# Performance work log

Measured on AMD Instinct MI355X. Metric: run time of the kernel, lower is better.

Reference implementation:

```python
import jax, jax.numpy as jnp
import numpy as np

DIM = 2048
NUM_HEADS = 16
NUM_KV_HEADS = 4
HEAD_DIM = DIM // NUM_HEADS  # 128
ROPE_BASE = 10000.0
CLIP = 31.0
BLOCK = 128


def fake_quant(w):
    """Blockwise int-ish fake quantization, steady QAT state (ratio=1, clip=31, no noise)."""
    out_f, in_f = w.shape
    pad = (-in_f) % BLOCK
    wp = jnp.pad(w, ((0, 0), (0, pad)))
    wb = wp.reshape(-1, BLOCK)
    # scale computed under no_grad in torch -> stop_gradient
    bmax = jnp.max(jnp.abs(wb), axis=1)
    s = jnp.maximum(bmax / CLIP, 1e-12).astype(jnp.float16)
    s = jnp.maximum(s, jnp.finfo(jnp.float16).tiny).astype(jnp.float32)
    s = jax.lax.stop_gradient(s)[:, None]
    ws = wb / s
    q = ws - jax.lax.stop_gradient(ws) + jax.lax.stop_gradient(
        jnp.round(jnp.clip(ws, -(CLIP + 1.0), CLIP)))  # STE
    qw = (q * s).reshape(out_f, in_f + pad)
    return qw[:, :in_f] if pad > 0 else qw


def rms_norm(x):
    eps = jnp.finfo(x.dtype).eps
    return x * jax.lax.rsqrt(jnp.mean(x * x, axis=-1, keepdims=True) + eps)


def rope_tables(seqlen, dtype):
    inv_freq = 1.0 / (ROPE_BASE ** (jnp.arange(0, HEAD_DIM, 2, dtype=jnp.float32) / HEAD_DIM))
    freqs = jnp.outer(jnp.arange(seqlen, dtype=jnp.float32), inv_freq)  # [S, hd/2]
    return jnp.cos(freqs).astype(dtype), jnp.sin(freqs).astype(dtype)


def apply_rotary(x, cos, sin):
    # x: [B,H,S,hd]; cos/sin: [S,hd/2]
    half = x.shape[-1] // 2
    x1, x2 = x[..., :half], x[..., half:]
    return jnp.concatenate((x1 * cos + x2 * sin, -x1 * sin + x2 * cos), axis=-1)


def setup_inputs() -> dict:
    key = jax.random.key(0)
    ks = jax.random.split(key, 6)
    kv_dim = NUM_KV_HEADS * HEAD_DIM
    std = DIM ** -0.5
    return {
        "x": jax.random.normal(ks[0], (2, 2048, DIM), dtype=jnp.float32),
        "Wq": jax.random.normal(ks[1], (DIM, DIM), dtype=jnp.float32) * std,
        "Wk": jax.random.normal(ks[2], (kv_dim, DIM), dtype=jnp.float32) * std,
        "Wv": jax.random.normal(ks[3], (kv_dim, DIM), dtype=jnp.float32) * std,
        "Wproj": jax.random.normal(ks[4], (DIM, DIM), dtype=jnp.float32) * std,
        "q_gain": jnp.full((NUM_HEADS,), 1.0, dtype=jnp.float32),
    }


def reference(x, Wq, Wk, Wv, Wproj, q_gain):
    B, S, D = x.shape
    H, KV, hd = NUM_HEADS, NUM_KV_HEADS, HEAD_DIM
    q = (x @ fake_quant(Wq).T).reshape(B, S, H, hd).transpose(0, 2, 1, 3)   # [B,H,S,hd]
    k = (x @ fake_quant(Wk).T).reshape(B, S, KV, hd).transpose(0, 2, 1, 3)  # [B,KV,S,hd]
    v = (x @ fake_quant(Wv).T).reshape(B, S, KV, hd).transpose(0, 2, 1, 3)
    q = rms_norm(q)
    k = rms_norm(k)
    cos, sin = rope_tables(S, q.dtype)
    q = apply_rotary(q, cos, sin)
    k = apply_rotary(k, cos, sin)
    q = q * q_gain[None, :, None, None]
    # GQA: expand kv heads
    rep = H // KV
    k = jnp.repeat(k, rep, axis=1)  # [B,H,S,hd]
    v = jnp.repeat(v, rep, axis=1)
    scale = 1.0 / jnp.sqrt(jnp.asarray(hd, dtype=q.dtype))
    scores = jnp.einsum("bhqd,bhkd->bhqk", q, k) * scale
    causal = jnp.tril(jnp.ones((S, S), dtype=bool))
    scores = jnp.where(causal, scores, jnp.asarray(-jnp.inf, dtype=scores.dtype))
    attn = jax.nn.softmax(scores, axis=-1)
    y = jnp.einsum("bhqk,bhkd->bhqd", attn, v)  # [B,H,S,hd]
    y = y.transpose(0, 2, 1, 3).reshape(B, S, D)
    return y @ fake_quant(Wproj).T
```

## Files before the change

kernel.cpp:

```cpp
#include <hip/hip_runtime.h>
#include <hip/hip_bf16.h>
#include <hip/hip_fp16.h>

#define SEQ    2048
#define DMODEL 2048
#define NH     16
#define NKV    4
#define HD     128
#define NTOT   3072
#define MROWS  4096

typedef __attribute__((ext_vector_type(4))) float f32x4;
typedef __attribute__((ext_vector_type(8))) __bf16 bf16x8;
typedef __attribute__((ext_vector_type(8))) unsigned short u16x8;
typedef __attribute__((ext_vector_type(4))) unsigned short u16x4;

__device__ __forceinline__ void async_copy16(const void* g, void* l) {
  __builtin_amdgcn_global_load_lds(
      (const __attribute__((address_space(1))) void*)g,
      (__attribute__((address_space(3))) void*)l, 16, 0, 0);
}

__device__ __forceinline__ unsigned short fto16(float f) {
  __hip_bfloat16 h = __float2bfloat16(f);
  return *(unsigned short*)&h;
}

__device__ __forceinline__ float b2f(unsigned short u) {
  unsigned int t = (unsigned int)u << 16;
  float f;
  __builtin_memcpy(&f, &t, 4);
  return f;
}

#define QSCALE 0.12751791437524245f
#define NEG_L2RB_64 (-0.2076205059304601f)

#define NFQ   20480
#define NCONV 8192
#define NROPE 512
__global__ __launch_bounds__(256) void prep_kernel(const float* __restrict__ Wq,
                                                   const float* __restrict__ Wk,
                                                   const float* __restrict__ Wv,
                                                   const float* __restrict__ Wp,
                                                   const float* __restrict__ x,
                                                   unsigned short* __restrict__ Wcat,
                                                   unsigned short* __restrict__ Wpq,
                                                   unsigned short* __restrict__ xb,
                                                   float* __restrict__ CS,
                                                   float* __restrict__ SN) {
  const int bid = blockIdx.x;
  const int tid = threadIdx.x;
  if (bid < NFQ) {
    int g = bid * 4 + (tid >> 6);
    int lane = tid & 63;
    const float* W;
    unsigned short* out;
    int blk;
    if (g < 32768)      { W = Wq; out = Wcat;                          blk = g; }
    else if (g < 40960) { W = Wk; out = Wcat + (size_t)2048 * 2048;    blk = g - 32768; }
    else if (g < 49152) { W = Wv; out = Wcat + (size_t)2560 * 2048;    blk = g - 40960; }
    else                { W = Wp; out = Wpq;                           blk = g - 49152; }
    const float* p = W + (size_t)blk * 128 + lane * 2;
    float w0 = p[0], w1 = p[1];
    float m = fmaxf(fabsf(w0), fabsf(w1));
#pragma unroll
    for (int o = 32; o; o >>= 1) m = fmaxf(m, __shfl_xor(m, o));
    float s = fmaxf(m / 31.0f, 1e-12f);
    s = __half2float(__float2half(s));
    s = fmaxf(s, 6.103515625e-05f);
    float q0 = rintf(fminf(fmaxf(w0 / s, -32.0f), 31.0f)) * s;
    float q1 = rintf(fminf(fmaxf(w1 / s, -32.0f), 31.0f)) * s;
    unsigned short* o16 = out + (size_t)blk * 128 + lane * 2;
    o16[0] = fto16(q0);
    o16[1] = fto16(q1);
  } else if (bid < NFQ + NCONV) {
    int i = ((bid - NFQ) * 256 + tid) * 4;
    float4 v = *(const float4*)(x + i);
    ushort4 o;
    o.x = fto16(v.x); o.y = fto16(v.y); o.z = fto16(v.z); o.w = fto16(v.w);
    *(ushort4*)(xb + i) = o;
  } else {
    int idx = (bid - NFQ - NCONV) * 256 + tid;
    int t = idx >> 6, l = idx & 63;
    float invf = exp2f((float)l * NEG_L2RB_64);
    float fr = (float)t * invf;
    CS[idx] = cosf(fr);
    SN[idx] = sinf(fr);
  }
}

#define BM 128
#define BN 128
#define BK 64
template <typename OT, bool FUSED>
__global__ __launch_bounds__(256, 3) void gemm_bt(const unsigned short* __restrict__ A,
                                                  const unsigned short* __restrict__ Bm,
                                                  OT* __restrict__ C,
                                                  unsigned short* __restrict__ vtb,
                                                  unsigned short* __restrict__ qbuf,
                                                  unsigned short* __restrict__ kbuf,
                                                  const float* __restrict__ qgain,
                                                  const float* __restrict__ CS,
                                                  const float* __restrict__ SN,
                                                  int M, int N, int K) {
  __shared__ unsigned short SH[FUSED ? 16896 : 16384];
  unsigned short* As = SH;
  unsigned short* Bs = SH + 8192;
  const int tid = threadIdx.x;
  const int wave = tid >> 6, lane = tid & 63;
  const int quad = lane >> 4, l16 = lane & 15;

  int wg = blockIdx.y * gridDim.x + blockIdx.x;
  int nwg = gridDim.x * gridDim.y;
  int cpx = nwg >> 3;
  int swz = (wg & 7) * cpx + (wg >> 3);
  int bxs = swz % gridDim.x, bys = swz / gridDim.x;
  const int m0 = bxs * BM, n0 = bys * BN;
  const int wm = (wave >> 1) * 64, wn = (wave & 1) * 64;

  const unsigned short* Ag = A + (size_t)m0 * K;
  const unsigned short* Bg = Bm + (size_t)n0 * K;

  f32x4 acc[4][4];
#pragma unroll
  for (int i = 0; i < 4; i++)
#pragma unroll
    for (int j = 0; j < 4; j++) acc[i][j] = f32x4{0.f, 0.f, 0.f, 0.f};

  const int srow = tid >> 3;
  const int sg8 = (((lane & 7) ^ (lane >> 3))) * 8;
  const unsigned short* gA = Ag + (size_t)srow * K + sg8;
  const unsigned short* gB = Bg + (size_t)srow * K + sg8;
  unsigned short* lA = &As[wave * 512];
  unsigned short* lB = &Bs[wave * 512];

  for (int k0 = 0; k0 < K; k0 += BK) {
    __syncthreads();
#pragma unroll
    for (int c = 0; c < 4; ++c) async_copy16(gA + (size_t)c * 32 * K + k0, lA + c * 2048);
#pragma unroll
    for (int c = 0; c < 4; ++c) async_copy16(gB + (size_t)c * 32 * K + k0, lB + c * 2048);
    __syncthreads();
#pragma unroll
    for (int kk = 0; kk < 2; ++kk) {
      bf16x8 af[4], bf[4];
#pragma unroll
      for (int t = 0; t < 4; t++)
        af[t] = *(const bf16x8*)&As[(wm + t * 16 + l16) * BK + ((((kk << 2) + quad) ^ (l16 & 7)) << 3)];
#pragma unroll
      for (int t = 0; t < 4; t++)
        bf[t] = *(const bf16x8*)&Bs[(wn + t * 16 + l16) * BK + ((((kk << 2) + quad) ^ (l16 & 7)) << 3)];
#pragma unroll
      for (int i = 0; i < 4; i++)
#pragma unroll
        for (int j = 0; j < 4; j++)
          acc[i][j] = __builtin_amdgcn_mfma_f32_16x16x32_bf16(af[i], bf[j], acc[i][j], 0, 0, 0);
    }
  }

  if constexpr (FUSED) {
    if (n0 >= 2560) {
      const int kvh = (n0 - 2560) >> 7;
#pragma unroll
      for (int i = 0; i < 4; i++) {
        int row0 = m0 + wm + i * 16 + quad * 4;
        int bz = row0 >> 11, s0 = row0 & 2047;
#pragma unroll
        for (int j = 0; j < 4; j++) {
          int d = wn + j * 16 + l16;
          u16x4 o;
#pragma unroll
          for (int r = 0; r < 4; r++) o[r] = fto16(acc[i][j][r]);
          *(u16x4*)&vtb[(size_t)((bz * NKV + kvh) * HD + d) * SEQ + s0] = o;
        }
      }
      return;
    }
    __syncthreads();
#pragma unroll
    for (int i = 0; i < 4; i++) {
      int tok0 = wm + i * 16 + quad * 4;
#pragma unroll
      for (int j = 0; j < 4; j++) {
        int d = wn + j * 16 + l16;
        u16x4 w;
#pragma unroll
        for (int r = 0; r < 4; r++) w[r] = fto16(acc[i][j][r]);
        *(u16x4*)&SH[d * 132 + tok0] = w;
      }
    }
    __syncthreads();
    const bool isq = (n0 < 2048);
    const int hh = isq ? (n0 >> 7) : ((n0 - 2048) >> 7);
    const float g = isq ? qgain[hh] * QSCALE : 1.0f;
#pragma unroll 1
    for (int gr = 0; gr < 8; ++gr) {
      int tk = wave * 32 + gr * 4;
      u16x4 a = *(const u16x4*)&SH[lane * 132 + tk];
      u16x4 b = *(const u16x4*)&SH[(lane + 64) * 132 + tk];
      float x1[4], x2[4], ss[4];
#pragma unroll
      for (int r = 0; r < 4; r++) {
        x1[r] = b2f(a[r]); x2[r] = b2f(b[r]);
        ss[r] = x1[r] * x1[r] + x2[r] * x2[r];
      }
#pragma unroll
      for (int o = 32; o; o >>= 1)
#pragma unroll
        for (int r = 0; r < 4; r++) ss[r] += __shfl_xor(ss[r], o);
#pragma unroll
      for (int r = 0; r < 4; r++) {
        int gt = m0 + tk + r;
        int bz = gt >> 11, tokg = gt & 2047;
        float rn = rsqrtf(ss[r] * (1.0f / 128.0f) + 1.1920929e-07f);
        float cs = CS[tokg * 64 + lane], sn = SN[tokg * 64 + lane];
        float n1 = x1[r] * rn, n2 = x2[r] * rn;
        unsigned short* dst = isq
            ? qbuf + ((size_t)(bz * NH + hh) * SEQ + tokg) * HD
            : kbuf + ((size_t)(bz * NKV + hh) * SEQ + tokg) * HD;
        dst[lane]      = fto16((n1 * cs + n2 * sn) * g);
        dst[lane + 64] = fto16((-n1 * sn + n2 * cs) * g);
      }
    }
    return;
  }

#pragma unroll
  for (int i = 0; i < 4; i++) {
    int row_base = m0 + wm + i * 16 + quad * 4;
#pragma unroll
    for (int j = 0; j < 4; j++) {
      int col = n0 + wn + j * 16 + l16;
#pragma unroll
      for (int r = 0; r < 4; r++) {
        if constexpr (sizeof(OT) == 2)
          C[(size_t)(row_base + r) * N + col] = fto16(acc[i][j][r]);
        else
          C[(size_t)(row_base + r) * N + col] = acc[i][j][r];
      }
    }
  }
}

__global__ __launch_bounds__(512, 4) void attn_kernel(const unsigned short* __restrict__ qb,
                                                      const unsigned short* __restrict__ kb,
                                                      const unsigned short* __restrict__ vtb,
                                                      unsigned short* __restrict__ yb,
                                                      float* __restrict__ Opart,
                                                      float* __restrict__ mlb) {
  __shared__ unsigned short Ks[2][64 * 128];
  __shared__ unsigned short Vt[128 * 64];
  __shared__ unsigned short Ps[8][16 * 64];

  const int bx = blockIdx.x;
  const int h = blockIdx.y;
  const int bz = blockIdx.z;
  const int tid = threadIdx.x;
  const int wave = tid >> 6, lane = tid & 63;
  const int quad = lane >> 4, l16 = lane & 15;

  int qt, k0, k1, cchunk = -1, qi = 0;
  if (bx < 12) {
    qt = bz ? bx : (11 - bx);
    k0 = 0; k1 = 2 * qt + 2;
  } else {
    int idx = bx - 12;
    qi = idx >> 1; cchunk = idx & 1;
    qt = 12 + qi;
    int nkt = 2 * qt + 2, half = nkt >> 1;
    k0 = cchunk ? half : 0;
    k1 = cchunk ? nkt : half;
  }

  const int base = qt * 128 + wave * 16;
  const int kdiag = base >> 6;

  const unsigned short* qg = qb + (size_t)(bz * NH + h) * SEQ * HD;
  const unsigned short* kg = kb + (size_t)(bz * NKV + (h >> 2)) * SEQ * HD;
  const unsigned short* vg = vtb + (size_t)(bz * NKV + (h >> 2)) * HD * SEQ;
  unsigned short* psw = &Ps[wave][0];

  bf16x8 qf[4];
#pragma unroll
  for (int ds = 0; ds < 4; ++ds)
    qf[ds] = *(const bf16x8*)(qg + (size_t)(base + l16) * HD + ds * 32 + quad * 8);

  f32x4 oacc[8];
#pragma unroll
  for (int j = 0; j < 8; ++j) oacc[j] = f32x4{0.f, 0.f, 0.f, 0.f};
  float m_i = -__builtin_inff();
  float l_i = 0.f;

  const int krow0 = wave * 4 + (lane >> 4);
  const int ksrcg = (lane & 15) ^ (krow0 & 15);
  const unsigned short* kgK = kg + (size_t)krow0 * HD + ksrcg * 8;

  const int vdw = tid >> 3, vgr = tid & 7;

  async_copy16(kgK + (size_t)k0 * 64 * HD, &Ks[k0 & 1][wave * 512]);
  async_copy16(kgK + (size_t)(k0 * 64 + 32) * HD, &Ks[k0 & 1][4096 + wave * 512]);
  u16x8 pv[2];
#pragma unroll
  for (int i = 0; i < 2; ++i)
    pv[i] = *(const u16x8*)(vg + (size_t)(i * 64 + vdw) * SEQ + k0 * 64 + vgr * 8);

  for (int kt = k0; kt < k1; ++kt) {
    __syncthreads();
#pragma unroll
    for (int i = 0; i < 2; ++i) {
      int d = i * 64 + vdw;
      *(u16x8*)&Vt[d * 64 + ((vgr ^ (d & 7)) << 3)] = pv[i];
    }
    if (kt + 1 < k1) {
      const unsigned short* s = kgK + (size_t)(kt + 1) * 64 * HD;
      async_copy16(s, &Ks[(kt + 1) & 1][wave * 512]);
      async_copy16(s + (size_t)32 * HD, &Ks[(kt + 1) & 1][4096 + wave * 512]);
    }
    __asm__ volatile("s_waitcnt lgkmcnt(0)" ::: "memory");
    __builtin_amdgcn_sched_barrier(0);
    __asm__ volatile("s_barrier" ::: "memory");

    if (kt + 1 < k1) {
#pragma unroll
      for (int i = 0; i < 2; ++i)
        pv[i] = *(const u16x8*)(vg + (size_t)(i * 64 + vdw) * SEQ + (kt + 1) * 64 + vgr * 8);
    }

    if (kt <= kdiag) {
      const unsigned short* Kc = Ks[kt & 1];
      f32x4 st[4];
#pragma unroll
      for (int mt = 0; mt < 4; ++mt) st[mt] = f32x4{0.f, 0.f, 0.f, 0.f};
      __builtin_amdgcn_s_setprio(1);
#pragma unroll
      for (int mt = 0; mt < 4; ++mt)
#pragma unroll
        for (int ds = 0; ds < 4; ++ds) {
          bf16x8 kf = *(const bf16x8*)&Kc[(mt * 16 + l16) * 128 + ((((ds << 2) + quad) ^ l16) << 3)];
          st[mt] = __builtin_amdgcn_mfma_f32_16x16x32_bf16(kf, qf[ds], st[mt], 0, 0, 0);
        }
      __builtin_amdgcn_s_setprio(0);

      const int qrow = base + l16;
      float p[4][4];
      float mx = -__builtin_inff();
      if (kt == kdiag) {
#pragma unroll
        for (int mt = 0; mt < 4; ++mt)
#pragma unroll
          for (int r = 0; r < 4; ++r) {
            int kp = kt * 64 + mt * 16 + quad * 4 + r;
            float v = (kp <= qrow) ? st[mt][r] : -__builtin_inff();
            p[mt][r] = v;
            mx = fmaxf(mx, v);
          }
      } else {
#pragma unroll
        for (int mt = 0; mt < 4; ++mt)
#pragma unroll
          for (int r = 0; r < 4; ++r) {
            p[mt][r] = st[mt][r];
            mx = fmaxf(mx, st[mt][r]);
          }
      }
      mx = fmaxf(mx, __shfl_xor(mx, 16));
      mx = fmaxf(mx, __shfl_xor(mx, 32));
      float mnew = (mx > m_i + 8.f) ? mx : m_i;
      float rs = 0.f;
#pragma unroll
      for (int mt = 0; mt < 4; ++mt)
#pragma unroll
        for (int r = 0; r < 4; ++r) {
          float e = exp2f(p[mt][r] - mnew);
          p[mt][r] = e;
          rs += e;
        }
      rs += __shfl_xor(rs, 16);
      rs += __shfl_xor(rs, 32);
      if (mnew != m_i) {
        float a = exp2f(m_i - mnew);
#pragma unroll
        for (int j = 0; j < 8; ++j) oacc[j] *= a;
        l_i = l_i * a + rs;
        m_i = mnew;
      } else {
        l_i += rs;
      }

#pragma unroll
      for (int mt = 0; mt < 4; ++mt) {
        u16x4 w;
#pragma unroll
        for (int r = 0; r < 4; ++r) w[r] = fto16(p[mt][r]);
        int g = mt * 2 + (quad >> 1);
        *(u16x4*)&psw[l16 * 64 + ((g ^ (l16 & 7)) << 3) + (quad & 1) * 4] = w;
      }

      __asm__ volatile("s_waitcnt lgkmcnt(0)" ::: "memory");

      __builtin_amdgcn_s_setprio(1);
#pragma unroll
      for (int c = 0; c < 2; ++c) {
        bf16x8 pf = *(const bf16x8*)&psw[l16 * 64 + ((((c << 2) + quad) ^ (l16 & 7)) << 3)];
#pragma unroll
        for (int mt = 0; mt < 8; ++mt) {
          bf16x8 vf = *(const bf16x8*)&Vt[(mt * 16 + l16) * 64 + ((((c << 2) + quad) ^ (l16 & 7)) << 3)];
          oacc[mt] = __builtin_amdgcn_mfma_f32_16x16x32_bf16(vf, pf, oacc[mt], 0, 0, 0);
        }
      }
      __builtin_amdgcn_s_setprio(0);
    }
  }

  if (cchunk >= 0) {
    const int rloc = wave * 16 + l16;
    float* op = Opart + ((size_t)(((cchunk * 2 + bz) * NH + h) * 4 + qi) * 128 + rloc) * 128;
#pragma unroll
    for (int mt = 0; mt < 8; ++mt)
      *(f32x4*)&op[mt * 16 + quad * 4] = oacc[mt];
    if (quad == 0) {
      float* ml = mlb + (size_t)(((cchunk * 2 + bz) * NH + h) * 4 + qi) * 256;
      ml[rloc] = m_i;
      ml[128 + rloc] = l_i;
    }
    return;
  }

  {
    float il = 1.0f / l_i;
    int qrow = base + l16;
#pragma unroll
    for (int mt = 0; mt < 8; ++mt) {
      u16x4 o;
#pragma unroll
      for (int r = 0; r < 4; ++r) o[r] = fto16(oacc[mt][r] * il);
      *(u16x4*)&yb[(size_t)(bz * SEQ + qrow) * DMODEL + h * HD + mt * 16 + quad * 4] = o;
    }
  }
}

__global__ __launch_bounds__(256) void combine_kernel(const float* __restrict__ Opart,
                                                      const float* __restrict__ mlb,
                                                      unsigned short* __restrict__ yb) {
  const int qi = blockIdx.x & 3;
  const int h = (blockIdx.x >> 2) & 15;
  const int bz = blockIdx.x >> 6;
  const int q = threadIdx.x >> 1;
  const int dh = (threadIdx.x & 1) * 64;

  const size_t i0 = (size_t)(((0 * 2 + bz) * NH + h) * 4 + qi);
  const size_t i1 = (size_t)(((1 * 2 + bz) * NH + h) * 4 + qi);
  const float m1 = mlb[i0 * 256 + q],     l1 = mlb[i0 * 256 + 128 + q];
  const float m2 = mlb[i1 * 256 + q],     l2 = mlb[i1 * 256 + 128 + q];
  const float mm = fmaxf(m1, m2);
  float w1 = exp2f(m1 - mm), w2 = exp2f(m2 - mm);
  const float il = 1.0f / (l1 * w1 + l2 * w2);
  w1 *= il; w2 *= il;

  const float* o1 = Opart + (i0 * 128 + q) * 128;
  const float* o2 = Opart + (i1 * 128 + q) * 128;
  const int qrow = (12 + qi) * 128 + q;
  unsigned short* dst = yb + (size_t)(bz * SEQ + qrow) * DMODEL + h * HD;
#pragma unroll
  for (int d0 = 0; d0 < 64; d0 += 4) {
    f32x4 a = *(const f32x4*)&o1[dh + d0];
    f32x4 b = *(const f32x4*)&o2[dh + d0];
    u16x4 o;
#pragma unroll
    for (int r = 0; r < 4; ++r) o[r] = fto16(a[r] * w1 + b[r] * w2);
    *(u16x4*)&dst[dh + d0] = o;
  }
}

extern "C" void kernel_launch(void* const* d_in, const int* in_sizes, int n_in,
                              void* d_out, int out_size, void* d_ws, size_t ws_size,
                              hipStream_t stream) {
  (void)in_sizes; (void)n_in; (void)out_size; (void)ws_size;
  const float* x  = (const float*)d_in[0];
  const float* Wq = (const float*)d_in[1];
  const float* Wk = (const float*)d_in[2];
  const float* Wv = (const float*)d_in[3];
  const float* Wp = (const float*)d_in[4];
  const float* qg = (const float*)d_in[5];
  float* out = (float*)d_out;
  char* ws = (char*)d_ws;

  unsigned short* xb   = (unsigned short*)(ws + 0);
  unsigned short* Wcat = (unsigned short*)(ws + 16777216);
  unsigned short* Wpq  = (unsigned short*)(ws + 29360128);
  float*          CS   = (float*)(ws + 37748736);
  float*          SN   = (float*)(ws + 38273024);
  float*          Opart= (float*)(ws + 38797312);
  float*          mlb  = (float*)(ws + 55574528);
  unsigned short* qbuf = (unsigned short*)(ws + 62914560);
  unsigned short* kbuf = (unsigned short*)(ws + 79691776);
  unsigned short* vtb  = (unsigned short*)(ws + 83886080);
  unsigned short* yb   = xb;

  prep_kernel<<<NFQ + NCONV + NROPE, 256, 0, stream>>>(Wq, Wk, Wv, Wp, x,
                                                       Wcat, Wpq, xb, CS, SN);
  gemm_bt<unsigned short, true><<<dim3(32, 24), 256, 0, stream>>>(
      xb, Wcat, (unsigned short*)nullptr, vtb, qbuf, kbuf, qg, CS, SN,
      MROWS, NTOT, DMODEL);
  attn_kernel<<<dim3(20, NH, 2), 512, 0, stream>>>(qbuf, kbuf, vtb, yb, Opart, mlb);
  combine_kernel<<<128, 256, 0, stream>>>(Opart, mlb, yb);
  gemm_bt<float, false><<<dim3(32, 16), 256, 0, stream>>>(
      yb, Wpq, out, nullptr, nullptr, nullptr, nullptr, nullptr, nullptr,
      MROWS, DMODEL, DMODEL);
}
```

Baseline: 307.5 us.

## Pair short and long causal query tiles per block to balance attention work

Rebalances the causal attention work distribution. Blocks 0-3 now each process two query tiles in sequence, a long one (7-bx) and a short one (bx), giving a balanced amount of key-tile work. Tiles 8-11 run alone and tiles 12-15 stay split in two for the combine kernel. The grid shrinks from 20 to 16 blocks in x, which cuts tail imbalance and block count. The cost is a serialized two-segment loop with an extra sync and reload, and one fewer wave of blocks in flight.

```diff
diff --git a/kernel.cpp b/kernel.cpp
--- a/kernel.cpp
+++ b/kernel.cpp
@@ -260,182 +260,187 @@
   const int wave = tid >> 6, lane = tid & 63;
   const int quad = lane >> 4, l16 = lane & 15;
 
-  int qt, k0, k1, cchunk = -1, qi = 0;
-  if (bx < 12) {
-    qt = bz ? bx : (11 - bx);
-    k0 = 0; k1 = 2 * qt + 2;
+  int nseg = 1, qtS[2], k0S[2], k1S[2], cchunk = -1, qi = 0;
+  if (bx < 4) {
+    nseg = 2;
+    qtS[0] = 7 - bx; k0S[0] = 0; k1S[0] = 2 * (7 - bx) + 2;
+    qtS[1] = bx;     k0S[1] = 0; k1S[1] = 2 * bx + 2;
+  } else if (bx < 8) {
+    qtS[0] = bx + 4; k0S[0] = 0; k1S[0] = 2 * (bx + 4) + 2;
   } else {
-    int idx = bx - 12;
+    int idx = bx - 8;
     qi = idx >> 1; cchunk = idx & 1;
-    qt = 12 + qi;
-    int nkt = 2 * qt + 2, half = nkt >> 1;
-    k0 = cchunk ? half : 0;
-    k1 = cchunk ? nkt : half;
-  }
-
-  const int base = qt * 128 + wave * 16;
-  const int kdiag = base >> 6;
+    int qt = 12 + qi, half = qt + 1;
+    qtS[0] = qt;
+    k0S[0] = cchunk ? half : 0;
+    k1S[0] = cchunk ? (2 * qt + 2) : half;
+  }
 
   const unsigned short* qg = qb + (size_t)(bz * NH + h) * SEQ * HD;
   const unsigned short* kg = kb + (size_t)(bz * NKV + (h >> 2)) * SEQ * HD;
   const unsigned short* vg = vtb + (size_t)(bz * NKV + (h >> 2)) * HD * SEQ;
   unsigned short* psw = &Ps[wave][0];
 
-  bf16x8 qf[4];
-#pragma unroll
-  for (int ds = 0; ds < 4; ++ds)
-    qf[ds] = *(const bf16x8*)(qg + (size_t)(base + l16) * HD + ds * 32 + quad * 8);
-
-  f32x4 oacc[8];
-#pragma unroll
-  for (int j = 0; j < 8; ++j) oacc[j] = f32x4{0.f, 0.f, 0.f, 0.f};
-  float m_i = -__builtin_inff();
-  float l_i = 0.f;
-
   const int krow0 = wave * 4 + (lane >> 4);
   const int ksrcg = (lane & 15) ^ (krow0 & 15);
   const unsigned short* kgK = kg + (size_t)krow0 * HD + ksrcg * 8;
-
   const int vdw = tid >> 3, vgr = tid & 7;
 
-  async_copy16(kgK + (size_t)k0 * 64 * HD, &Ks[k0 & 1][wave * 512]);
-  async_copy16(kgK + (size_t)(k0 * 64 + 32) * HD, &Ks[k0 & 1][4096 + wave * 512]);
-  u16x8 pv[2];
-#pragma unroll
-  for (int i = 0; i < 2; ++i)
-    pv[i] = *(const u16x8*)(vg + (size_t)(i * 64 + vdw) * SEQ + k0 * 64 + vgr * 8);
-
-  for (int kt = k0; kt < k1; ++kt) {
+#pragma unroll 1
+  for (int s = 0; s < nseg; ++s) {
+    const int qt = qtS[s], k0 = k0S[s], k1 = k1S[s];
+    const int base = qt * 128 + wave * 16;
+    const int kdiag = base >> 6;
+
     __syncthreads();
-#pragma unroll
-    for (int i = 0; i < 2; ++i) {
-      int d = i * 64 + vdw;
-      *(u16x8*)&Vt[d * 64 + ((vgr ^ (d & 7)) << 3)] = pv[i];
-    }
-    if (kt + 1 < k1) {
-      const unsigned short* s = kgK + (size_t)(kt + 1) * 64 * HD;
-      async_copy16(s, &Ks[(kt + 1) & 1][wave * 512]);
-      async_copy16(s + (size_t)32 * HD, &Ks[(kt + 1) & 1][4096 + wave * 512]);
-    }
-    __asm__ volatile("s_waitcnt lgkmcnt(0)" ::: "memory");
-    __builtin_amdgcn_sched_barrier(0);
-    __asm__ volatile("s_barrier" ::: "memory");
-
-    if (kt + 1 < k1) {
-#pragma unroll
-      for (int i = 0; i < 2; ++i)
-        pv[i] = *(const u16x8*)(vg + (size_t)(i * 64 + vdw) * SEQ + (kt + 1) * 64 + vgr * 8);
-    }
-
-    if (kt <= kdiag) {
-      const unsigned short* Kc = Ks[kt & 1];
-      f32x4 st[4];
-#pragma unroll
-      for (int mt = 0; mt < 4; ++mt) st[mt] = f32x4{0.f, 0.f, 0.f, 0.f};
-      __builtin_amdgcn_s_setprio(1);
-#pragma unroll
-      for (int mt = 0; mt < 4; ++mt)
-#pragma unroll
-        for (int ds = 0; ds < 4; ++ds) {
-          bf16x8 kf = *(const bf16x8*)&Kc[(mt * 16 + l16) * 128 + ((((ds << 2) + quad) ^ l16) << 3)];
-          st[mt] = __builtin_amdgcn_mfma_f32_16x16x32_bf16(kf, qf[ds], st[mt], 0, 0, 0);
+
+    async_copy16(kgK + (size_t)k0 * 64 * HD, &Ks[k0 & 1][wave * 512]);
+    async_copy16(kgK + (size_t)(k0 * 64 + 32) * HD, &Ks[k0 & 1][4096 + wave * 512]);
+    u16x8 pv[2];
+#pragma unroll
+    for (int i = 0; i < 2; ++i)
+      pv[i] = *(const u16x8*)(vg + (size_t)(i * 64 + vdw) * SEQ + k0 * 64 + vgr * 8);
+
+    bf16x8 qf[4];
+#pragma unroll
+    for (int ds = 0; ds < 4; ++ds)
+      qf[ds] = *(const bf16x8*)(qg + (size_t)(base + l16) * HD + ds * 32 + quad * 8);
+
+    f32x4 oacc[8];
+#pragma unroll
+    for (int j = 0; j < 8; ++j) oacc[j] = f32x4{0.f, 0.f, 0.f, 0.f};
+    float m_i = -__builtin_inff();
+    float l_i = 0.f;
+
+    for (int kt = k0; kt < k1; ++kt) {
+      __syncthreads();
+#pragma unroll
+      for (int i = 0; i < 2; ++i) {
+        int d = i * 64 + vdw;
+        *(u16x8*)&Vt[d * 64 + ((vgr ^ (d & 7)) << 3)] = pv[i];
+      }
+      if (kt + 1 < k1) {
+        const unsigned short* sp = kgK + (size_t)(kt + 1) * 64 * HD;
+        async_copy16(sp, &Ks[(kt + 1) & 1][wave * 512]);
+        async_copy16(sp + (size_t)32 * HD, &Ks[(kt + 1) & 1][4096 + wave * 512]);
+      }
+      __asm__ volatile("s_waitcnt lgkmcnt(0)" ::: "memory");
+      __builtin_amdgcn_sched_barrier(0);
+      __asm__ volatile("s_barrier" ::: "memory");
+
+      if (kt + 1 < k1) {
+#pragma unroll
+        for (int i = 0; i < 2; ++i)
+          pv[i] = *(const u16x8*)(vg + (size_t)(i * 64 + vdw) * SEQ + (kt + 1) * 64 + vgr * 8);
+      }
+
+      if (kt <= kdiag) {
+        const unsigned short* Kc = Ks[kt & 1];
+        f32x4 st[4];
+#pragma unroll
+        for (int mt = 0; mt < 4; ++mt) st[mt] = f32x4{0.f, 0.f, 0.f, 0.f};
+        __builtin_amdgcn_s_setprio(1);
+#pragma unroll
+        for (int mt = 0; mt < 4; ++mt)
+#pragma unroll
+          for (int ds = 0; ds < 4; ++ds) {
+            bf16x8 kf = *(const bf16x8*)&Kc[(mt * 16 + l16) * 128 + ((((ds << 2) + quad) ^ l16) << 3)];
+            st[mt] = __builtin_amdgcn_mfma_f32_16x16x32_bf16(kf, qf[ds], st[mt], 0, 0, 0);
+          }
+        __builtin_amdgcn_s_setprio(0);
+
+        const int qrow = base + l16;
+        float p[4][4];
+        float mx = -__builtin_inff();
+        if (kt == kdiag) {
+#pragma unroll
+          for (int mt = 0; mt < 4; ++mt)
+#pragma unroll
+            for (int r = 0; r < 4; ++r) {
+              int kp = kt * 64 + mt * 16 + quad * 4 + r;
+              float v = (kp <= qrow) ? st[mt][r] : -__builtin_inff();
+              p[mt][r] = v;
+              mx = fmaxf(mx, v);
+            }
+        } else {
+#pragma unroll
+          for (int mt = 0; mt < 4; ++mt)
+#pragma unroll
+            for (int r = 0; r < 4; ++r) {
+              p[mt][r] = st[mt][r];
+              mx = fmaxf(mx, st[mt][r]);
+            }
         }
-      __builtin_amdgcn_s_setprio(0);
-
-      const int qrow = base + l16;
-      float p[4][4];
-      float mx = -__builtin_inff();
-      if (kt == kdiag) {
+        mx = fmaxf(mx, __shfl_xor(mx, 16));
+        mx = fmaxf(mx, __shfl_xor(mx, 32));
+        float mnew = (mx > m_i + 8.f) ? mx : m_i;
+        float rs = 0.f;
 #pragma unroll
         for (int mt = 0; mt < 4; ++mt)
 #pragma unroll
           for (int r = 0; r < 4; ++r) {
-            int kp = kt * 64 + mt * 16 + quad * 4 + r;
-            float v = (kp <= qrow) ? st[mt][r] : -__builtin_inff();
-            p[mt][r] = v;
-            mx = fmaxf(mx, v);
+            float e = exp2f(p[mt][r] - mnew);
+            p[mt][r] = e;
+            rs += e;
           }
-      } else {
-#pragma unroll
-        for (int mt = 0; mt < 4; ++mt)
-#pragma unroll
-          for (int r = 0; r < 4; ++r) {
-            p[mt][r] = st[mt][r];
-            mx = fmaxf(mx, st[mt][r]);
+        rs += __shfl_xor(rs, 16);
+        rs += __shfl_xor(rs, 32);
+        if (mnew != m_i) {
+          float a = exp2f(m_i - mnew);
+#pragma unroll
+          for (int j = 0; j < 8; ++j) oacc[j] *= a;
+          l_i = l_i * a + rs;
+          m_i = mnew;
+        } else {
+          l_i += rs;
+        }
+
+#pragma unroll
+        for (int mt = 0; mt < 4; ++mt) {
+          u16x4 w;
+#pragma unroll
+          for (int r = 0; r < 4; ++r) w[r] = fto16(p[mt][r]);
+          int g = mt * 2 + (quad >> 1);
+          *(u16x4*)&psw[l16 * 64 + ((g ^ (l16 & 7)) << 3) + (quad & 1) * 4] = w;
+        }
+
+        __asm__ volatile("s_waitcnt lgkmcnt(0)" ::: "memory");
+
+        __builtin_amdgcn_s_setprio(1);
+#pragma unroll
+        for (int c = 0; c < 2; ++c) {
+          bf16x8 pf = *(const bf16x8*)&psw[l16 * 64 + ((((c << 2) + quad) ^ (l16 & 7)) << 3)];
+#pragma unroll
+          for (int mt = 0; mt < 8; ++mt) {
+            bf16x8 vf = *(const bf16x8*)&Vt[(mt * 16 + l16) * 64 + ((((c << 2) + quad) ^ (l16 & 7)) << 3)];
+            oacc[mt] = __builtin_amdgcn_mfma_f32_16x16x32_bf16(vf, pf, oacc[mt], 0, 0, 0);
           }
-      }
-      mx = fmaxf(mx, __shfl_xor(mx, 16));
-      mx = fmaxf(mx, __shfl_xor(mx, 32));
-      float mnew = (mx > m_i + 8.f) ? mx : m_i;
-      float rs = 0.f;
-#pragma unroll
-      for (int mt = 0; mt < 4; ++mt)
-#pragma unroll
-        for (int r = 0; r < 4; ++r) {
-          float e = exp2f(p[mt][r] - mnew);
-          p[mt][r] = e;
-          rs += e;
         }
-      rs += __shfl_xor(rs, 16);
-      rs += __shfl_xor(rs, 32);
-      if (mnew != m_i) {
-        float a = exp2f(m_i - mnew);
-#pragma unroll
-        for (int j = 0; j < 8; ++j) oacc[j] *= a;
-        l_i = l_i * a + rs;
-        m_i = mnew;
-      } else {
-        l_i += rs;
-      }
-
-#pragma unroll
-      for (int mt = 0; mt < 4; ++mt) {
-        u16x4 w;
-#pragma unroll
-        for (int r = 0; r < 4; ++r) w[r] = fto16(p[mt][r]);
-        int g = mt * 2 + (quad >> 1);
-        *(u16x4*)&psw[l16 * 64 + ((g ^ (l16 & 7)) << 3) + (quad & 1) * 4] = w;
-      }
-
-      __asm__ volatile("s_waitcnt lgkmcnt(0)" ::: "memory");
-
-      __builtin_amdgcn_s_setprio(1);
-#pragma unroll
-      for (int c = 0; c < 2; ++c) {
-        bf16x8 pf = *(const bf16x8*)&psw[l16 * 64 + ((((c << 2) + quad) ^ (l16 & 7)) << 3)];
-#pragma unroll
-        for (int mt = 0; mt < 8; ++mt) {
-          bf16x8 vf = *(const bf16x8*)&Vt[(mt * 16 + l16) * 64 + ((((c << 2) + quad) ^ (l16 & 7)) << 3)];
-          oacc[mt] = __builtin_amdgcn_mfma_f32_16x16x32_bf16(vf, pf, oacc[mt], 0, 0, 0);
-        }
-      }
-      __builtin_amdgcn_s_setprio(0);
-    }
-  }
-
-  if (cchunk >= 0) {
-    const int rloc = wave * 16 + l16;
-    float* op = Opart + ((size_t)(((cchunk * 2 + bz) * NH + h) * 4 + qi) * 128 + rloc) * 128;
-#pragma unroll
-    for (int mt = 0; mt < 8; ++mt)
-      *(f32x4*)&op[mt * 16 + quad * 4] = oacc[mt];
-    if (quad == 0) {
-      float* ml = mlb + (size_t)(((cchunk * 2 + bz) * NH + h) * 4 + qi) * 256;
-      ml[rloc] = m_i;
-      ml[128 + rloc] = l_i;
-    }
-    return;
-  }
-
-  {
-    float il = 1.0f / l_i;
-    int qrow = base + l16;
-#pragma unroll
-    for (int mt = 0; mt < 8; ++mt) {
-      u16x4 o;
-#pragma unroll
-      for (int r = 0; r < 4; ++r) o[r] = fto16(oacc[mt][r] * il);
-      *(u16x4*)&yb[(size_t)(bz * SEQ + qrow) * DMODEL + h * HD + mt * 16 + quad * 4] = o;
+        __builtin_amdgcn_s_setprio(0);
+      }
+    }
+
+    if (cchunk >= 0) {
+      const int rloc = wave * 16 + l16;
+      float* op = Opart + ((size_t)(((cchunk * 2 + bz) * NH + h) * 4 + qi) * 128 + rloc) * 128;
+#pragma unroll
+      for (int mt = 0; mt < 8; ++mt)
+        *(f32x4*)&op[mt * 16 + quad * 4] = oacc[mt];
+      if (quad == 0) {
+        float* ml = mlb + (size_t)(((cchunk * 2 + bz) * NH + h) * 4 + qi) * 256;
+        ml[rloc] = m_i;
+        ml[128 + rloc] = l_i;
+      }
+    } else {
+      float il = 1.0f / l_i;
+      int qrow = base + l16;
+#pragma unroll
+      for (int mt = 0; mt < 8; ++mt) {
+        u16x4 o;
+#pragma unroll
+        for (int r = 0; r < 4; ++r) o[r] = fto16(oacc[mt][r] * il);
+        *(u16x4*)&yb[(size_t)(bz * SEQ + qrow) * DMODEL + h * HD + mt * 16 + quad * 4] = o;
+      }
     }
   }
 }
@@ -503,7 +508,7 @@
   gemm_bt<unsigned short, true><<<dim3(32, 24), 256, 0, stream>>>(
       xb, Wcat, (unsigned short*)nullptr, vtb, qbuf, kbuf, qg, CS, SN,
       MROWS, NTOT, DMODEL);
-  attn_kernel<<<dim3(20, NH, 2), 512, 0, stream>>>(qbuf, kbuf, vtb, yb, Opart, mlb);
+  attn_kernel<<<dim3(16, NH, 2), 512, 0, stream>>>(qbuf, kbuf, vtb, yb, Opart, mlb);
   combine_kernel<<<128, 256, 0, stream>>>(Opart, mlb, yb);
   gemm_bt<float, false><<<dim3(32, 16), 256, 0, stream>>>(
       yb, Wpq, out, nullptr, nullptr, nullptr, nullptr, nullptr, nullptr,
```

After: 308.5 us. About the same (+0.3%).
